# Kernel optimization log

Measured on AMD Instinct MI355X. Metric: run time of the kernel, lower is better.

Reference implementation:

```python
import jax, jax.numpy as jnp
import numpy as np

N = 50000      # nodes
E = 800000     # edges (avg degree 16)
IN = 256       # in_dim == heads*hidden (so DGL residual is Identity)
H = 4          # heads
D = 64         # hidden_dim / out_dim per head
EPS = 1e-5
NEG_SLOPE_ATTN = 0.2   # DGL GATConv edge-attention leaky_relu slope
NEG_SLOPE_ACT = 0.01   # F.leaky_relu default


def gat_conv(x, src, dst, W, al, ar, b, act):
    # x: [N, H*D], W: [H*D, H*D], al/ar: [H, D], b: [H*D]
    feat = (x @ W).reshape(N, H, D)                       # [N,H,D]
    el = jnp.sum(feat * al, axis=-1)                      # [N,H]
    er = jnp.sum(feat * ar, axis=-1)                      # [N,H]
    e = jax.nn.leaky_relu(el[src] + er[dst], NEG_SLOPE_ATTN)  # [E,H]
    # segment softmax over incoming edges per destination node
    m = jax.ops.segment_max(e, dst, num_segments=N)       # [N,H]
    m = jnp.where(jnp.isfinite(m), m, 0.0)                # nodes with no in-edges
    ee = jnp.exp(e - m[dst])                              # [E,H]
    denom = jax.ops.segment_sum(ee, dst, num_segments=N)  # [N,H]
    alpha = ee / jnp.maximum(denom[dst], 1e-9)            # [E,H]
    msg = feat[src] * alpha[:, :, None]                   # [E,H,D]
    rst = jax.ops.segment_sum(msg, dst, num_segments=N)   # [N,H,D]
    rst = rst + x.reshape(N, H, D)                        # identity residual (dims match)
    rst = rst + b.reshape(1, H, D)
    if act:
        rst = jax.nn.leaky_relu(rst, NEG_SLOPE_ACT)
    return rst


def batch_norm(h, gamma, beta):
    # BatchNorm1d in training mode: batch statistics over node dim
    mu = jnp.mean(h, axis=0)
    var = jnp.var(h, axis=0)
    return (h - mu) * jax.lax.rsqrt(var + EPS) * gamma + beta


def setup_inputs():
    key = jax.random.key(0)
    ks = jax.random.split(key, 18)
    s = 1.0 / np.sqrt(IN)
    inp = {
        'x': jax.random.normal(ks[0], (N, IN), jnp.float32),
        'src': jax.random.randint(ks[1], (E,), 0, N),
        'dst': jax.random.randint(ks[2], (E,), 0, N),
    }
    names = ['W1', 'al1', 'ar1', 'b1', 'W2', 'al2', 'ar2', 'b2', 'W3', 'al3', 'ar3', 'b3']
    shapes = [(IN, H * D), (H, D), (H, D), (H * D,)] * 3
    for i, (nm, sh) in enumerate(zip(names, shapes)):
        inp[nm] = jax.random.normal(ks[3 + i], sh, jnp.float32) * s
    inp['g1'] = jnp.ones((H * D,), jnp.float32)
    inp['be1'] = jnp.zeros((H * D,), jnp.float32)
    inp['g2'] = jnp.ones((H * D,), jnp.float32)
    inp['be2'] = jnp.zeros((H * D,), jnp.float32)
    return inp


def reference(x, src, dst, W1, al1, ar1, b1, W2, al2, ar2, b2, W3, al3, ar3, b3, g1, be1, g2, be2):
    h = gat_conv(x, src, dst, W1, al1, ar1, b1, act=True).reshape(N, H * D)
    h = batch_norm(h, g1, be1)
    h = gat_conv(h, src, dst, W2, al2, ar2, b2, act=True).reshape(N, H * D)
    h = batch_norm(h, g2, be2)
    h = gat_conv(h, src, dst, W3, al3, ar3, b3, act=False)   # [N,H,D]
    return h.mean(axis=1)                                    # [N,D]
```

## Files before the change

### kernel.cpp

```cpp
#include <hip/hip_runtime.h>

constexpr int NN = 50000;
constexpr int NE = 800000;
constexpr float SLOPE_A = 0.2f;
constexpr float SLOPE_R = 0.01f;
constexpr int SCB = 196;

typedef __attribute__((ext_vector_type(8))) short bf16x8;
typedef __attribute__((ext_vector_type(4))) float f32x4;

__device__ __forceinline__ unsigned short f2bf(float f) {
    union { float f; unsigned u; } v; v.f = f;
    unsigned u = v.u;
    unsigned r = u + 0x7fffu + ((u >> 16) & 1u);
    return (unsigned short)(r >> 16);
}
__device__ __forceinline__ float bf2f(unsigned short s) {
    union { unsigned u; float f; } v; v.u = ((unsigned)s) << 16;
    return v.f;
}

__global__ void k_hist(const int* __restrict__ dst, int* __restrict__ cnt) {
    int i = blockIdx.x * 256 + threadIdx.x;
    if (i < NE) atomicAdd(&cnt[dst[i]], 1);
}

__global__ void k_scan1(const int* __restrict__ cnt, int* __restrict__ loc,
                        int* __restrict__ bsum) {
    __shared__ int sh[256];
    int t = threadIdx.x;
    int i = blockIdx.x * 256 + t;
    int v = (i < NN) ? cnt[i] : 0;
    sh[t] = v;
    __syncthreads();
    for (int off = 1; off < 256; off <<= 1) {
        int tmp = (t >= off) ? sh[t - off] : 0;
        __syncthreads();
        sh[t] += tmp;
        __syncthreads();
    }
    loc[i] = sh[t] - v;
    if (t == 255) bsum[blockIdx.x] = sh[255];
}

__global__ void k_scan2(const int* __restrict__ bsum, int* __restrict__ boff,
                        int* __restrict__ rowptr) {
    __shared__ int sh[256];
    int t = threadIdx.x;
    int v = (t < SCB) ? bsum[t] : 0;
    sh[t] = v;
    __syncthreads();
    for (int off = 1; off < 256; off <<= 1) {
        int tmp = (t >= off) ? sh[t - off] : 0;
        __syncthreads();
        sh[t] += tmp;
        __syncthreads();
    }
    if (t < SCB) boff[t] = sh[t] - v;
    if (t == 255) rowptr[NN] = sh[255];
}

__global__ void k_scan3(const int* __restrict__ loc, const int* __restrict__ boff,
                        int* __restrict__ rowptr, int* __restrict__ cursor) {
    int i = blockIdx.x * 256 + threadIdx.x;
    if (i < NN) {
        int r = loc[i] + boff[blockIdx.x];
        rowptr[i] = r;
        cursor[i] = r;
    }
}

__global__ void k_scatter(const int* __restrict__ src, const int* __restrict__ dst,
                          int* __restrict__ cursor, int* __restrict__ ssrc) {
    int i = blockIdx.x * 256 + threadIdx.x;
    if (i < NE) {
        int d = dst[i];
        int pos = atomicAdd(&cursor[d], 1);
        ssrc[pos] = src[i];
    }
}

__global__ void k_prepw(const float* __restrict__ W1, const float* __restrict__ W2,
                        const float* __restrict__ W3, unsigned short* __restrict__ Wt) {
    int b = blockIdx.x;
    int L = b >> 8, k = b & 255;
    const float* W = (L == 0) ? W1 : ((L == 1) ? W2 : W3);
    int j = threadIdx.x;
    Wt[L * 65536 + j * 256 + k] = f2bf(W[k * 256 + j]);
}

__global__ void k_fold(const unsigned short* __restrict__ Wt, const float* __restrict__ sc,
                       const float* __restrict__ sh, unsigned short* __restrict__ Wfrag,
                       float* __restrict__ cvec) {
    int b = blockIdx.x;
    if (b < 512) {
        int gid = b * 256 + threadIdx.x;
        int lane = gid & 63;
        int frag = gid >> 6;
        int j = frag & 3, kc = (frag >> 2) & 7, w = frag >> 5;
        int mm = lane & 15, q = lane >> 4;
        int n = 64 * w + 16 * j + mm;
        int k0 = kc * 32 + q * 8;
        const unsigned short* srcp = Wt + n * 256 + k0;
        unsigned short o[8];
        if (sc) {
#pragma unroll
            for (int t = 0; t < 8; t++)
                o[t] = f2bf(sc[k0 + t] * bf2f(srcp[t]));
        } else {
#pragma unroll
            for (int t = 0; t < 8; t++) o[t] = srcp[t];
        }
        *(uint4*)(Wfrag + (size_t)gid * 8) = *(const uint4*)o;
    } else {
        __shared__ float red[256];
        int n = b - 512;
        int k = threadIdx.x;
        red[k] = sh[k] * bf2f(Wt[n * 256 + k]);
        __syncthreads();
        for (int off = 128; off > 0; off >>= 1) {
            if (k < off) red[k] += red[k + off];
            __syncthreads();
        }
        if (k == 0) cvec[n] = red[0];
    }
}

__launch_bounds__(256, 2)
__global__ void k_gemm(const void* __restrict__ Araw, int af32,
                       const unsigned short* __restrict__ Wfrag,
                       const float* __restrict__ cvec,
                       const float* __restrict__ al, const float* __restrict__ ar,
                       unsigned short* __restrict__ feat16, float* __restrict__ el,
                       float* __restrict__ er) {
    constexpr int AP = 264;
    __shared__ __align__(16) unsigned short Alds[64 * AP];
    const int tid = threadIdx.x;
    const int rowbase = blockIdx.x * 64;

    if (af32) {
        const float* A = (const float*)Araw;
        int r = tid >> 6;
        int c4 = tid & 63;
        for (int it = 0; it < 16; it++) {
            int rr = it * 4 + r;
            int gr = rowbase + rr;
            float4 v = make_float4(0.f, 0.f, 0.f, 0.f);
            if (gr < NN) v = *(const float4*)(A + (size_t)gr * 256 + c4 * 4);
            ushort4 pv;
            pv.x = f2bf(v.x); pv.y = f2bf(v.y); pv.z = f2bf(v.z); pv.w = f2bf(v.w);
            *(ushort4*)(&Alds[rr * AP + c4 * 4]) = pv;
        }
    } else {
        const unsigned short* A = (const unsigned short*)Araw;
        for (int it = 0; it < 8; it++) {
            int idx = it * 256 + tid;
            int rr = idx >> 5;
            int c16 = idx & 31;
            int gr = rowbase + rr;
            uint4 v = make_uint4(0u, 0u, 0u, 0u);
            if (gr < NN) v = *(const uint4*)(A + (size_t)gr * 256 + c16 * 8);
            *(uint4*)(&Alds[rr * AP + c16 * 8]) = v;
        }
    }
    __syncthreads();

    f32x4 acc[4][4];
    for (int i = 0; i < 4; i++)
        for (int j = 0; j < 4; j++)
            acc[i][j] = (f32x4){0.f, 0.f, 0.f, 0.f};

    const int lane = tid & 63, w = tid >> 6;
    const int mm = lane & 15, q = lane >> 4;

    const unsigned short* bbase = Wfrag + ((size_t)w * 8 * 4) * 512 + (size_t)lane * 8;

#pragma unroll
    for (int kc = 0; kc < 8; kc++) {
        bf16x8 a[4], b[4];
        for (int i = 0; i < 4; i++)
            a[i] = *(const bf16x8*)(&Alds[(16 * i + mm) * AP + kc * 32 + q * 8]);
        for (int j = 0; j < 4; j++)
            b[j] = *(const bf16x8*)(bbase + (size_t)(kc * 4 + j) * 512);
        for (int i = 0; i < 4; i++)
            for (int j = 0; j < 4; j++)
                acc[i][j] = __builtin_amdgcn_mfma_f32_16x16x32_bf16(a[i], b[j], acc[i][j], 0, 0, 0);
    }
    __syncthreads();

    if (cvec) {
        float cv[4];
        for (int j = 0; j < 4; j++) cv[j] = cvec[64 * w + 16 * j + mm];
        for (int i = 0; i < 4; i++)
            for (int j = 0; j < 4; j++)
                for (int r = 0; r < 4; r++)
                    acc[i][j][r] += cv[j];
    }

    float alv[4], arv[4];
    for (int j = 0; j < 4; j++) {
        alv[j] = al[w * 64 + 16 * j + mm];
        arv[j] = ar[w * 64 + 16 * j + mm];
    }
    for (int i = 0; i < 4; i++) {
        for (int r = 0; r < 4; r++) {
            int gr = rowbase + 16 * i + q * 4 + r;
            float se = 0.f, sr = 0.f;
            for (int j = 0; j < 4; j++) {
                se += acc[i][j][r] * alv[j];
                sr += acc[i][j][r] * arv[j];
            }
            for (int off = 1; off < 16; off <<= 1) {
                se += __shfl_xor(se, off, 64);
                sr += __shfl_xor(sr, off, 64);
            }
            if (mm == 0 && gr < NN) {
                el[gr * 4 + w] = se;
                er[gr * 4 + w] = sr;
            }
        }
    }

    for (int i = 0; i < 4; i++)
        for (int j = 0; j < 4; j++) {
            int gc = 64 * w + 16 * j + mm;
            for (int r = 0; r < 4; r++) {
                int rr = 16 * i + q * 4 + r;
                Alds[rr * AP + gc] = f2bf(acc[i][j][r]);
            }
        }
    __syncthreads();
    for (int it = 0; it < 8; it++) {
        int idx = it * 256 + tid;
        int rr = idx >> 5;
        int c16 = idx & 31;
        int gr = rowbase + rr;
        if (gr < NN)
            *(uint4*)(feat16 + (size_t)gr * 256 + c16 * 8) = *(const uint4*)(&Alds[rr * AP + c16 * 8]);
    }
}

__launch_bounds__(256)
__global__ void k_agg(const unsigned short* __restrict__ feat16, const float* __restrict__ el,
                      const float* __restrict__ er, const int* __restrict__ rowptr,
                      const int* __restrict__ ssrc,
                      const unsigned short* __restrict__ residh, const float* __restrict__ residf,
                      const float* __restrict__ bnscale, const float* __restrict__ bnshift,
                      int use_bn, const float* __restrict__ bias, int act,
                      unsigned short* __restrict__ outh, float* __restrict__ outf,
                      int final_mean) {
    __shared__ float comb[2][64][5];
    int tid = threadIdx.x;
    int nl = tid >> 7;
    int v = (tid >> 6) & 1;
    int l = tid & 63;
    int n = __builtin_amdgcn_readfirstlane(blockIdx.x * 2 + nl);
    int h = l >> 4;
    int beg = rowptr[n], end = rowptr[n + 1];
    float erh = er[n * 4 + h];

    float d = 0.f;
    float4 acc = make_float4(0.f, 0.f, 0.f, 0.f);

    for (int e = beg + 8 * v; e < end; e += 16) {
        int ss[8];
        float cc[8];
        ushort4 ff[8];
#pragma unroll
        for (int j = 0; j < 8; j++) {
            int ee = e + j;
            ss[j] = ssrc[(ee < end) ? ee : beg];
        }
#pragma unroll
        for (int j = 0; j < 8; j++)
            cc[j] = el[ss[j] * 4 + h];
#pragma unroll
        for (int j = 0; j < 8; j++)
            ff[j] = *(const ushort4*)(feat16 + (size_t)ss[j] * 256 + l * 4);
#pragma unroll
        for (int j = 0; j < 8; j++) {
            float sc = cc[j] + erh;
            sc = (sc > 0.f) ? sc : SLOPE_A * sc;
            float wgt = ((e + j) < end) ? __expf(sc) : 0.f;
            d += wgt;
            acc.x += bf2f(ff[j].x) * wgt;
            acc.y += bf2f(ff[j].y) * wgt;
            acc.z += bf2f(ff[j].z) * wgt;
            acc.w += bf2f(ff[j].w) * wgt;
        }
    }

    if (v == 1) {
        comb[nl][l][0] = acc.x; comb[nl][l][1] = acc.y;
        comb[nl][l][2] = acc.z; comb[nl][l][3] = acc.w;
        comb[nl][l][4] = d;
    }
    __syncthreads();
    if (v == 1) return;
    acc.x += comb[nl][l][0]; acc.y += comb[nl][l][1];
    acc.z += comb[nl][l][2]; acc.w += comb[nl][l][3];
    d += comb[nl][l][4];

    float invd = 1.f / fmaxf(d, 1e-9f);
    acc.x *= invd; acc.y *= invd; acc.z *= invd; acc.w *= invd;

    float4 r;
    if (residf) {
        r = *(const float4*)(residf + (size_t)n * 256 + l * 4);
    } else {
        ushort4 rv = *(const ushort4*)(residh + (size_t)n * 256 + l * 4);
        r = make_float4(bf2f(rv.x), bf2f(rv.y), bf2f(rv.z), bf2f(rv.w));
    }
    if (use_bn) {
        float4 sc4 = *(const float4*)(bnscale + l * 4);
        float4 sh4 = *(const float4*)(bnshift + l * 4);
        r.x = r.x * sc4.x + sh4.x;
        r.y = r.y * sc4.y + sh4.y;
        r.z = r.z * sc4.z + sh4.z;
        r.w = r.w * sc4.w + sh4.w;
    }
    float4 bb = *(const float4*)(bias + l * 4);
    acc.x += r.x + bb.x; acc.y += r.y + bb.y;
    acc.z += r.z + bb.z; acc.w += r.w + bb.w;
    if (act) {
        acc.x = (acc.x > 0.f) ? acc.x : SLOPE_R * acc.x;
        acc.y = (acc.y > 0.f) ? acc.y : SLOPE_R * acc.y;
        acc.z = (acc.z > 0.f) ? acc.z : SLOPE_R * acc.z;
        acc.w = (acc.w > 0.f) ? acc.w : SLOPE_R * acc.w;
    }

    if (!final_mean) {
        ushort4 p;
        p.x = f2bf(acc.x); p.y = f2bf(acc.y); p.z = f2bf(acc.z); p.w = f2bf(acc.w);
        *(ushort4*)(outh + (size_t)n * 256 + l * 4) = p;
    } else {
        acc.x += __shfl_xor(acc.x, 16, 64); acc.x += __shfl_xor(acc.x, 32, 64);
        acc.y += __shfl_xor(acc.y, 16, 64); acc.y += __shfl_xor(acc.y, 32, 64);
        acc.z += __shfl_xor(acc.z, 16, 64); acc.z += __shfl_xor(acc.z, 32, 64);
        acc.w += __shfl_xor(acc.w, 16, 64); acc.w += __shfl_xor(acc.w, 32, 64);
        if (l < 16) {
            acc.x *= 0.25f; acc.y *= 0.25f; acc.z *= 0.25f; acc.w *= 0.25f;
            *(float4*)(outf + (size_t)n * 64 + l * 4) = acc;
        }
    }
}

__global__ void k_bnstats(const unsigned short* __restrict__ hh, float* __restrict__ sums) {
    int t = threadIdx.x;
    int b = blockIdx.x;
    int r0 = b * 196, r1 = min(r0 + 196, NN);
    float s = 0.f, s2 = 0.f;
    for (int r = r0; r < r1; r++) {
        float v = bf2f(hh[(size_t)r * 256 + t]);
        s += v; s2 += v * v;
    }
    atomicAdd(&sums[t], s);
    atomicAdd(&sums[256 + t], s2);
}

__global__ void k_bnfinal(const float* __restrict__ sums, const float* __restrict__ g,
                          const float* __restrict__ be, float* __restrict__ scale,
                          float* __restrict__ shift) {
    int t = threadIdx.x;
    float mu = sums[t] * (1.f / NN);
    float var = sums[256 + t] * (1.f / NN) - mu * mu;
    float rs = rsqrtf(var + 1e-5f);
    float sc = rs * g[t];
    scale[t] = sc;
    shift[t] = be[t] - mu * sc;
}

extern "C" void kernel_launch(void* const* d_in, const int* in_sizes, int n_in,
                              void* d_out, int out_size, void* d_ws, size_t ws_size,
                              hipStream_t stream) {
    const float* x   = (const float*)d_in[0];
    const int* src   = (const int*)d_in[1];
    const int* dst   = (const int*)d_in[2];
    const float* W1  = (const float*)d_in[3];
    const float* al1 = (const float*)d_in[4];
    const float* ar1 = (const float*)d_in[5];
    const float* b1  = (const float*)d_in[6];
    const float* W2  = (const float*)d_in[7];
    const float* al2 = (const float*)d_in[8];
    const float* ar2 = (const float*)d_in[9];
    const float* b2  = (const float*)d_in[10];
    const float* W3  = (const float*)d_in[11];
    const float* al3 = (const float*)d_in[12];
    const float* ar3 = (const float*)d_in[13];
    const float* b3  = (const float*)d_in[14];
    const float* g1  = (const float*)d_in[15];
    const float* be1 = (const float*)d_in[16];
    const float* g2  = (const float*)d_in[17];
    const float* be2 = (const float*)d_in[18];
    float* out = (float*)d_out;

    char* ws = (char*)d_ws;
    size_t off = 0;
    auto alloc = [&](size_t bytes) {
        void* p = ws + off;
        off += (bytes + 255) & ~(size_t)255;
        return p;
    };
    int* rowptr = (int*)alloc((NN + 1) * sizeof(int));
    int* cursor = (int*)alloc(NN * sizeof(int));
    int* cnt    = (int*)alloc(SCB * 256 * sizeof(int));
    int* loc    = (int*)alloc(SCB * 256 * sizeof(int));
    int* bsum   = (int*)alloc(SCB * sizeof(int));
    int* boff   = (int*)alloc(SCB * sizeof(int));
    int* ssrc   = (int*)alloc(NE * sizeof(int));
    unsigned short* feat16 = (unsigned short*)alloc((size_t)NN * 256 * sizeof(unsigned short));
    unsigned short* hbuf   = (unsigned short*)alloc((size_t)NN * 256 * sizeof(unsigned short));
    float* el   = (float*)alloc((size_t)NN * 4 * sizeof(float));
    float* er   = (float*)alloc((size_t)NN * 4 * sizeof(float));
    unsigned short* Wt     = (unsigned short*)alloc(3 * 65536 * sizeof(unsigned short));
    unsigned short* Wfrag1 = (unsigned short*)alloc(131072 * sizeof(unsigned short) * 8);
    unsigned short* Wfrag2 = (unsigned short*)alloc(131072 * sizeof(unsigned short) * 8);
    float* cvec    = (float*)alloc(256 * sizeof(float));
    float* bnsums  = (float*)alloc(512 * sizeof(float));
    float* bnscale = (float*)alloc(256 * sizeof(float));
    float* bnshift = (float*)alloc(256 * sizeof(float));

    hipMemsetAsync(cnt, 0, NN * sizeof(int), stream);
    k_hist<<<(NE + 255) / 256, 256, 0, stream>>>(dst, cnt);
    k_scan1<<<SCB, 256, 0, stream>>>(cnt, loc, bsum);
    k_scan2<<<1, 256, 0, stream>>>(bsum, boff, rowptr);
    k_scan3<<<SCB, 256, 0, stream>>>(loc, boff, rowptr, cursor);
    k_scatter<<<(NE + 255) / 256, 256, 0, stream>>>(src, dst, cursor, ssrc);
    k_prepw<<<768, 256, 0, stream>>>(W1, W2, W3, Wt);
    k_fold<<<512, 256, 0, stream>>>(Wt, nullptr, nullptr, Wfrag1, nullptr);

    const int GB = (NN + 63) / 64;
    const int NB = NN / 2;

    k_gemm<<<GB, 256, 0, stream>>>(x, 1, Wfrag1, nullptr, al1, ar1, feat16, el, er);
    k_agg<<<NB, 256, 0, stream>>>(feat16, el, er, rowptr, ssrc, nullptr, x,
                                  nullptr, nullptr, 0, b1, 1, hbuf, nullptr, 0);
    hipMemsetAsync(bnsums, 0, 512 * sizeof(float), stream);
    k_bnstats<<<256, 256, 0, stream>>>(hbuf, bnsums);
    k_bnfinal<<<1, 256, 0, stream>>>(bnsums, g1, be1, bnscale, bnshift);
    k_fold<<<768, 256, 0, stream>>>(Wt + 65536, bnscale, bnshift, Wfrag2, cvec);

    k_gemm<<<GB, 256, 0, stream>>>(hbuf, 0, Wfrag2, cvec, al2, ar2, feat16, el, er);
    k_agg<<<NB, 256, 0, stream>>>(feat16, el, er, rowptr, ssrc, hbuf, nullptr,
                                  bnscale, bnshift, 1, b2, 1, hbuf, nullptr, 0);
    hipMemsetAsync(bnsums, 0, 512 * sizeof(float), stream);
    k_bnstats<<<256, 256, 0, stream>>>(hbuf, bnsums);
    k_bnfinal<<<1, 256, 0, stream>>>(bnsums, g2, be2, bnscale, bnshift);
    k_fold<<<768, 256, 0, stream>>>(Wt + 131072, bnscale, bnshift, Wfrag2, cvec);

    k_gemm<<<GB, 256, 0, stream>>>(hbuf, 0, Wfrag2, cvec, al3, ar3, feat16, el, er);
    k_agg<<<NB, 256, 0, stream>>>(feat16, el, er, rowptr, ssrc, hbuf, nullptr,
                                  bnscale, bnshift, 1, b3, 0, nullptr, out, 1);
}
```

Measured before the change: 610.1 us.

## Fold attention vectors into weights, single-wave agg per node, deterministic BN stats

Precomputes W·al and W·ar as an extra bf16 MFMA B-fragment, so el/er come from four extra MFMAs on wave 0 instead of per-row shuffle reductions. The fold kernel shrinks from 512 to 32 fragment blocks to match the actual fragment size. Aggregation drops to one wave per node with no LDS combine, giving four nodes per block. BN statistics switch from atomics to per-block partial sums reduced in bnfinal, which also removes the memsets. el/er are now computed from bf16-rounded folded weights, which adds some rounding error.

```diff
diff --git a/kernel.cpp b/kernel.cpp
--- a/kernel.cpp
+++ b/kernel.cpp
@@ -93,7 +93,7 @@
                        const float* __restrict__ sh, unsigned short* __restrict__ Wfrag,
                        float* __restrict__ cvec) {
     int b = blockIdx.x;
-    if (b < 512) {
+    if (b < 32) {
         int gid = b * 256 + threadIdx.x;
         int lane = gid & 63;
         int frag = gid >> 6;
@@ -114,7 +114,7 @@
         *(uint4*)(Wfrag + (size_t)gid * 8) = *(const uint4*)o;
     } else {
         __shared__ float red[256];
-        int n = b - 512;
+        int n = b - 32;
         int k = threadIdx.x;
         red[k] = sh[k] * bf2f(Wt[n * 256 + k]);
         __syncthreads();
@@ -126,11 +126,47 @@
     }
 }
 
+__global__ void k_foldlr(const unsigned short* __restrict__ Wt, const float* __restrict__ sc,
+                         const float* __restrict__ cvec, const float* __restrict__ al,
+                         const float* __restrict__ ar, unsigned short* __restrict__ wlrfrag,
+                         float* __restrict__ offlr) {
+    __shared__ float lw[256][8];
+    int k = threadIdx.x;
+    float scv = sc ? sc[k] : 1.f;
+    for (int h = 0; h < 4; h++) {
+        float sl = 0.f, sr = 0.f;
+        for (int d = 0; d < 64; d++) {
+            float wv = bf2f(Wt[(64 * h + d) * 256 + k]);
+            sl += wv * al[h * 64 + d];
+            sr += wv * ar[h * 64 + d];
+        }
+        lw[k][2 * h] = scv * sl;
+        lw[k][2 * h + 1] = scv * sr;
+    }
+    __syncthreads();
+    int kc = k >> 5, rem = k & 31, q = rem >> 3, t = rem & 7;
+    for (int mm = 0; mm < 16; mm++) {
+        unsigned short v = 0;
+        if (mm < 8) v = f2bf(lw[k][mm]);
+        wlrfrag[kc * 512 + (q * 16 + mm) * 8 + t] = v;
+    }
+    if (k < 8) {
+        float o = 0.f;
+        if (cvec) {
+            int h = k >> 1;
+            const float* a = (k & 1) ? ar : al;
+            for (int d = 0; d < 64; d++) o += cvec[64 * h + d] * a[h * 64 + d];
+        }
+        offlr[k] = o;
+    }
+}
+
 __launch_bounds__(256, 2)
 __global__ void k_gemm(const void* __restrict__ Araw, int af32,
                        const unsigned short* __restrict__ Wfrag,
                        const float* __restrict__ cvec,
-                       const float* __restrict__ al, const float* __restrict__ ar,
+                       const unsigned short* __restrict__ wlrfrag,
+                       const float* __restrict__ offlr,
                        unsigned short* __restrict__ feat16, float* __restrict__ el,
                        float* __restrict__ er) {
     constexpr int AP = 264;
@@ -169,6 +205,8 @@
     for (int i = 0; i < 4; i++)
         for (int j = 0; j < 4; j++)
             acc[i][j] = (f32x4){0.f, 0.f, 0.f, 0.f};
+    f32x4 accLR[4];
+    for (int i = 0; i < 4; i++) accLR[i] = (f32x4){0.f, 0.f, 0.f, 0.f};
 
     const int lane = tid & 63, w = tid >> 6;
     const int mm = lane & 15, q = lane >> 4;
@@ -185,6 +223,11 @@
         for (int i = 0; i < 4; i++)
             for (int j = 0; j < 4; j++)
                 acc[i][j] = __builtin_amdgcn_mfma_f32_16x16x32_bf16(a[i], b[j], acc[i][j], 0, 0, 0);
+        if (w == 0) {
+            bf16x8 blr = *(const bf16x8*)(wlrfrag + kc * 512 + lane * 8);
+            for (int i = 0; i < 4; i++)
+                accLR[i] = __builtin_amdgcn_mfma_f32_16x16x32_bf16(a[i], blr, accLR[i], 0, 0, 0);
+        }
     }
     __syncthreads();
 
@@ -197,28 +240,15 @@
                     acc[i][j][r] += cv[j];
     }
 
-    float alv[4], arv[4];
-    for (int j = 0; j < 4; j++) {
-        alv[j] = al[w * 64 + 16 * j + mm];
-        arv[j] = ar[w * 64 + 16 * j + mm];
-    }
-    for (int i = 0; i < 4; i++) {
-        for (int r = 0; r < 4; r++) {
-            int gr = rowbase + 16 * i + q * 4 + r;
-            float se = 0.f, sr = 0.f;
-            for (int j = 0; j < 4; j++) {
-                se += acc[i][j][r] * alv[j];
-                sr += acc[i][j][r] * arv[j];
+    if (w == 0 && mm < 8) {
+        float off = offlr[mm];
+        int h = mm >> 1;
+        float* dstp = (mm & 1) ? er : el;
+        for (int i = 0; i < 4; i++)
+            for (int r = 0; r < 4; r++) {
+                int gr = rowbase + 16 * i + q * 4 + r;
+                if (gr < NN) dstp[gr * 4 + h] = accLR[i][r] + off;
             }
-            for (int off = 1; off < 16; off <<= 1) {
-                se += __shfl_xor(se, off, 64);
-                sr += __shfl_xor(sr, off, 64);
-            }
-            if (mm == 0 && gr < NN) {
-                el[gr * 4 + w] = se;
-                er[gr * 4 + w] = sr;
-            }
-        }
     }
 
     for (int i = 0; i < 4; i++)
@@ -249,12 +279,8 @@
                       int use_bn, const float* __restrict__ bias, int act,
                       unsigned short* __restrict__ outh, float* __restrict__ outf,
                       int final_mean) {
-    __shared__ float comb[2][64][5];
-    int tid = threadIdx.x;
-    int nl = tid >> 7;
-    int v = (tid >> 6) & 1;
-    int l = tid & 63;
-    int n = __builtin_amdgcn_readfirstlane(blockIdx.x * 2 + nl);
+    int n = __builtin_amdgcn_readfirstlane(blockIdx.x * 4 + (threadIdx.x >> 6));
+    int l = threadIdx.x & 63;
     int h = l >> 4;
     int beg = rowptr[n], end = rowptr[n + 1];
     float erh = er[n * 4 + h];
@@ -262,7 +288,7 @@
     float d = 0.f;
     float4 acc = make_float4(0.f, 0.f, 0.f, 0.f);
 
-    for (int e = beg + 8 * v; e < end; e += 16) {
+    for (int e = beg; e < end; e += 8) {
         int ss[8];
         float cc[8];
         ushort4 ff[8];
@@ -289,17 +315,6 @@
             acc.w += bf2f(ff[j].w) * wgt;
         }
     }
-
-    if (v == 1) {
-        comb[nl][l][0] = acc.x; comb[nl][l][1] = acc.y;
-        comb[nl][l][2] = acc.z; comb[nl][l][3] = acc.w;
-        comb[nl][l][4] = d;
-    }
-    __syncthreads();
-    if (v == 1) return;
-    acc.x += comb[nl][l][0]; acc.y += comb[nl][l][1];
-    acc.z += comb[nl][l][2]; acc.w += comb[nl][l][3];
-    d += comb[nl][l][4];
 
     float invd = 1.f / fmaxf(d, 1e-9f);
     acc.x *= invd; acc.y *= invd; acc.z *= invd; acc.w *= invd;
@@ -345,25 +360,47 @@
     }
 }
 
-__global__ void k_bnstats(const unsigned short* __restrict__ hh, float* __restrict__ sums) {
-    int t = threadIdx.x;
-    int b = blockIdx.x;
+__global__ void k_bnstats(const unsigned short* __restrict__ hh, float* __restrict__ pbuf) {
+    __shared__ float ps[8 * 256];
+    __shared__ float ps2[8 * 256];
+    int t = threadIdx.x, b = blockIdx.x;
+    int r8 = t >> 5, c32 = t & 31;
     int r0 = b * 196, r1 = min(r0 + 196, NN);
-    float s = 0.f, s2 = 0.f;
-    for (int r = r0; r < r1; r++) {
-        float v = bf2f(hh[(size_t)r * 256 + t]);
-        s += v; s2 += v * v;
-    }
-    atomicAdd(&sums[t], s);
-    atomicAdd(&sums[256 + t], s2);
-}
-
-__global__ void k_bnfinal(const float* __restrict__ sums, const float* __restrict__ g,
+    float s[8], s2[8];
+#pragma unroll
+    for (int e = 0; e < 8; e++) { s[e] = 0.f; s2[e] = 0.f; }
+    for (int r = r0 + r8; r < r1; r += 8) {
+        uint4 v = *(const uint4*)(hh + (size_t)r * 256 + c32 * 8);
+        const unsigned short* pv = (const unsigned short*)&v;
+#pragma unroll
+        for (int e = 0; e < 8; e++) {
+            float f = bf2f(pv[e]);
+            s[e] += f; s2[e] += f * f;
+        }
+    }
+#pragma unroll
+    for (int e = 0; e < 8; e++) {
+        ps[r8 * 256 + c32 * 8 + e] = s[e];
+        ps2[r8 * 256 + c32 * 8 + e] = s2[e];
+    }
+    __syncthreads();
+    float ts = 0.f, ts2 = 0.f;
+    for (int g = 0; g < 8; g++) { ts += ps[g * 256 + t]; ts2 += ps2[g * 256 + t]; }
+    pbuf[b * 512 + t] = ts;
+    pbuf[b * 512 + 256 + t] = ts2;
+}
+
+__global__ void k_bnfinal(const float* __restrict__ pbuf, const float* __restrict__ g,
                           const float* __restrict__ be, float* __restrict__ scale,
                           float* __restrict__ shift) {
     int t = threadIdx.x;
-    float mu = sums[t] * (1.f / NN);
-    float var = sums[256 + t] * (1.f / NN) - mu * mu;
+    float s = 0.f, s2 = 0.f;
+    for (int b = 0; b < 256; b++) {
+        s += pbuf[b * 512 + t];
+        s2 += pbuf[b * 512 + 256 + t];
+    }
+    float mu = s * (1.f / NN);
+    float var = s2 * (1.f / NN) - mu * mu;
     float rs = rsqrtf(var + 1e-5f);
     float sc = rs * g[t];
     scale[t] = sc;
@@ -412,11 +449,13 @@
     unsigned short* hbuf   = (unsigned short*)alloc((size_t)NN * 256 * sizeof(unsigned short));
     float* el   = (float*)alloc((size_t)NN * 4 * sizeof(float));
     float* er   = (float*)alloc((size_t)NN * 4 * sizeof(float));
-    unsigned short* Wt     = (unsigned short*)alloc(3 * 65536 * sizeof(unsigned short));
-    unsigned short* Wfrag1 = (unsigned short*)alloc(131072 * sizeof(unsigned short) * 8);
-    unsigned short* Wfrag2 = (unsigned short*)alloc(131072 * sizeof(unsigned short) * 8);
+    unsigned short* Wt      = (unsigned short*)alloc(3 * 65536 * sizeof(unsigned short));
+    unsigned short* Wfrag1  = (unsigned short*)alloc(65536 * sizeof(unsigned short));
+    unsigned short* Wfrag2  = (unsigned short*)alloc(65536 * sizeof(unsigned short));
+    unsigned short* wlrfrag = (unsigned short*)alloc(4096 * sizeof(unsigned short));
+    float* offlr   = (float*)alloc(16 * sizeof(float));
     float* cvec    = (float*)alloc(256 * sizeof(float));
-    float* bnsums  = (float*)alloc(512 * sizeof(float));
+    float* pbuf    = (float*)alloc(256 * 512 * sizeof(float));
     float* bnscale = (float*)alloc(256 * sizeof(float));
     float* bnshift = (float*)alloc(256 * sizeof(float));
 
@@ -427,28 +466,29 @@
     k_scan3<<<SCB, 256, 0, stream>>>(loc, boff, rowptr, cursor);
     k_scatter<<<(NE + 255) / 256, 256, 0, stream>>>(src, dst, cursor, ssrc);
     k_prepw<<<768, 256, 0, stream>>>(W1, W2, W3, Wt);
-    k_fold<<<512, 256, 0, stream>>>(Wt, nullptr, nullptr, Wfrag1, nullptr);
+    k_fold<<<32, 256, 0, stream>>>(Wt, nullptr, nullptr, Wfrag1, nullptr);
+    k_foldlr<<<1, 256, 0, stream>>>(Wt, nullptr, nullptr, al1, ar1, wlrfrag, offlr);
 
     const int GB = (NN + 63) / 64;
-    const int NB = NN / 2;
-
-    k_gemm<<<GB, 256, 0, stream>>>(x, 1, Wfrag1, nullptr, al1, ar1, feat16, el, er);
+    const int NB = NN / 4;
+
+    k_gemm<<<GB, 256, 0, stream>>>(x, 1, Wfrag1, nullptr, wlrfrag, offlr, feat16, el, er);
     k_agg<<<NB, 256, 0, stream>>>(feat16, el, er, rowptr, ssrc, nullptr, x,
                                   nullptr, nullptr, 0, b1, 1, hbuf, nullptr, 0);
-    hipMemsetAsync(bnsums, 0, 512 * sizeof(float), stream);
-    k_bnstats<<<256, 256, 0, stream>>>(hbuf, bnsums);
-    k_bnfinal<<<1, 256, 0, stream>>>(bnsums, g1, be1, bnscale, bnshift);
-    k_fold<<<768, 256, 0, stream>>>(Wt + 65536, bnscale, bnshift, Wfrag2, cvec);
-
-    k_gemm<<<GB, 256, 0, stream>>>(hbuf, 0, Wfrag2, cvec, al2, ar2, feat16, el, er);
+    k_bnstats<<<256, 256, 0, stream>>>(hbuf, pbuf);
+    k_bnfinal<<<1, 256, 0, stream>>>(pbuf, g1, be1, bnscale, bnshift);
+    k_fold<<<288, 256, 0, stream>>>(Wt + 65536, bnscale, bnshift, Wfrag2, cvec);
+    k_foldlr<<<1, 256, 0, stream>>>(Wt + 65536, bnscale, cvec, al2, ar2, wlrfrag, offlr);
+
+    k_gemm<<<GB, 256, 0, stream>>>(hbuf, 0, Wfrag2, cvec, wlrfrag, offlr, feat16, el, er);
     k_agg<<<NB, 256, 0, stream>>>(feat16, el, er, rowptr, ssrc, hbuf, nullptr,
                                   bnscale, bnshift, 1, b2, 1, hbuf, nullptr, 0);
-    hipMemsetAsync(bnsums, 0, 512 * sizeof(float), stream);
-    k_bnstats<<<256, 256, 0, stream>>>(hbuf, bnsums);
-    k_bnfinal<<<1, 256, 0, stream>>>(bnsums, g2, be2, bnscale, bnshift);
-    k_fold<<<768, 256, 0, stream>>>(Wt + 131072, bnscale, bnshift, Wfrag2, cvec);
-
-    k_gemm<<<GB, 256, 0, stream>>>(hbuf, 0, Wfrag2, cvec, al3, ar3, feat16, el, er);
+    k_bnstats<<<256, 256, 0, stream>>>(hbuf, pbuf);
+    k_bnfinal<<<1, 256, 0, stream>>>(pbuf, g2, be2, bnscale, bnshift);
+    k_fold<<<288, 256, 0, stream>>>(Wt + 131072, bnscale, bnshift, Wfrag2, cvec);
+    k_foldlr<<<1, 256, 0, stream>>>(Wt + 131072, bnscale, cvec, al3, ar3, wlrfrag, offlr);
+
+    k_gemm<<<GB, 256, 0, stream>>>(hbuf, 0, Wfrag2, cvec, wlrfrag, offlr, feat16, el, er);
     k_agg<<<NB, 256, 0, stream>>>(feat16, el, er, rowptr, ssrc, hbuf, nullptr,
                                   bnscale, bnshift, 1, b3, 0, nullptr, out, 1);
 }
```

After: 577.2 us. 5.4% less time.
